# Kernel optimization log

Measured on AMD Instinct MI355X. Metric: run time of the kernel, lower is better.

Reference implementation:

```python
import jax, jax.numpy as jnp
import numpy as np

N_NODES = 60
N_EDGES = 1800
BATCH = 8192
NEG_SLOPE = 0.2  # PyG GATConv default leaky_relu slope


def _conv2d(x, w, b):
    y = jax.lax.conv_general_dilated(x, w, window_strides=(1, 1), padding='VALID',
                                     dimension_numbers=('NCHW', 'OIHW', 'NCHW'))
    return y + b[None, :, None, None]


def _maxpool2(x):
    return jax.lax.reduce_window(x, -jnp.inf, jax.lax.max, (1, 1, 2, 2), (1, 1, 2, 2), 'VALID')


def _gat(x, src, dst, edge_attr, W, a_src, a_dst, We, a_edge, b, n):
    # PyG GATConv, heads=1: xl = x W ; alpha_e = leakyrelu(a_src.xl[src] + a_dst.xl[dst] + a_edge.(edge_attr We))
    xl = x @ W                                    # [N, out]
    asrc = (xl * a_src).sum(-1)                   # [N]
    adst = (xl * a_dst).sum(-1)                   # [N]
    aedge = ((edge_attr @ We) * a_edge).sum(-1)   # [E]
    alpha = jax.nn.leaky_relu(asrc[src] + adst[dst] + aedge, NEG_SLOPE)
    # softmax over incoming edges of each dst node
    m = jax.ops.segment_max(alpha, dst, num_segments=n)
    ex = jnp.exp(alpha - m[dst])
    denom = jax.ops.segment_sum(ex, dst, num_segments=n)
    w_e = ex / denom[dst]
    out = jax.ops.segment_sum(w_e[:, None] * xl[src], dst, num_segments=n)
    return out + b


def _batchnorm_gnn(x):
    # torch code uses .item(): mean/std are detached python floats
    avg = jax.lax.stop_gradient(x.mean())
    std = jax.lax.stop_gradient(jnp.sqrt(((x - avg) ** 2).mean()))
    return (x - avg) / std


def setup_inputs() -> dict:
    key = jax.random.key(0)
    ks = jax.random.split(key, 24)
    f = lambda k, shape, scale=0.1: (jax.random.normal(k, shape, dtype=jnp.float32) * scale)
    inp = {
        'node_fea': jax.random.normal(ks[0], (N_NODES, 1), dtype=jnp.float32),
        'edge_fea': jax.random.normal(ks[1], (N_EDGES, 1), dtype=jnp.float32),
        'pic_fea': jax.random.normal(ks[2], (BATCH, 3, 32, 32), dtype=jnp.float32),
        'conv1_w': f(ks[3], (6, 3, 5, 5)), 'conv1_b': f(ks[4], (6,)),
        'conv2_w': f(ks[5], (16, 6, 5, 5)), 'conv2_b': f(ks[6], (16,)),
        'gat1_w': f(ks[7], (1, 6), 0.5), 'gat1_att_src': f(ks[8], (6,), 0.5),
        'gat1_att_dst': f(ks[9], (6,), 0.5), 'gat1_lin_edge': f(ks[10], (1, 6), 0.5),
        'gat1_att_edge': f(ks[11], (6,), 0.5), 'gat1_b': f(ks[12], (6,)),
        'gat2_w': f(ks[13], (6, 16), 0.3), 'gat2_att_src': f(ks[14], (16,), 0.3),
        'gat2_att_dst': f(ks[15], (16,), 0.3), 'gat2_lin_edge': f(ks[16], (1, 16), 0.3),
        'gat2_att_edge': f(ks[17], (16,), 0.3), 'gat2_b': f(ks[18], (16,)),
        'fc1_w': f(ks[19], (1360, 512), 0.03), 'fc1_b': f(ks[20], (512,)),
        'fc2_w': f(ks[21], (512, 10), 0.05), 'fc2_b': f(ks[22], (10,)),
        'edge_index': jax.random.randint(ks[23], (2, N_EDGES), 0, N_NODES, dtype=jnp.int64 if jax.config.jax_enable_x64 else jnp.int32),
    }
    return inp


def reference(node_fea, edge_fea, pic_fea,
              conv1_w, conv1_b, conv2_w, conv2_b,
              gat1_w, gat1_att_src, gat1_att_dst, gat1_lin_edge, gat1_att_edge, gat1_b,
              gat2_w, gat2_att_src, gat2_att_dst, gat2_lin_edge, gat2_att_edge, gat2_b,
              fc1_w, fc1_b, fc2_w, fc2_b, edge_index):
    n = node_fea.shape[0]
    # CNN branch: 32 -> 28 -> 14 -> 10 -> 5
    p = _maxpool2(jax.nn.relu(_conv2d(pic_fea, conv1_w, conv1_b)))
    p = _maxpool2(jax.nn.relu(_conv2d(p, conv2_w, conv2_b)))
    p = p.reshape(p.shape[0], -1)  # [B, 400]
    # add self loops (PyG default, fill_value='mean' for edge_attr)
    loop = jnp.arange(n)
    src = jnp.concatenate([edge_index[0], loop])
    dst = jnp.concatenate([edge_index[1], loop])
    ea = jnp.concatenate([edge_fea, jnp.broadcast_to(edge_fea.mean(0, keepdims=True), (n, edge_fea.shape[1]))], axis=0)
    # GNN branch
    x = _gat(node_fea, src, dst, ea, gat1_w, gat1_att_src, gat1_att_dst, gat1_lin_edge, gat1_att_edge, gat1_b, n)
    x = jax.nn.relu(_batchnorm_gnn(x))
    x = _gat(x, src, dst, ea, gat2_w, gat2_att_src, gat2_att_dst, gat2_lin_edge, gat2_att_edge, gat2_b, n)
    x = jax.nn.relu(_batchnorm_gnn(x))
    g = x.reshape(-1)  # [960]
    feat = jnp.concatenate([jnp.broadcast_to(g, (p.shape[0], g.shape[0])), p], axis=1)  # [B, 1360]
    h = jax.nn.relu(feat @ fc1_w + fc1_b)
    return jnp.tanh(h @ fc2_w + fc2_b)
```

## Files before the change

### kernel.cpp

```cpp
#include <hip/hip_runtime.h>
#include <math.h>

#define N_NODES 60
#define N_EDGES 1800
#define N_ETOT  1860
#define SLOPE   0.2f

struct ConvS {
    float simg[2 * 3 * 32 * 32];
    float c1[2 * 6 * 14 * 16];
    float pad[16];
};
struct GnnS {
    float ea[N_ETOT];
    float alpha[N_ETOT];
    float x_in[960];
    float xl[960];
    float outb[960];
    float as_[N_NODES], ad_[N_NODES], den_[N_NODES];
    float red[256];
    unsigned char srcs[N_ETOT], dsts[N_ETOT];
    unsigned short csr[N_ETOT];
    int cnt[N_NODES], off[N_NODES + 4];
};
union SMem { ConvS c; GnnS g; };

__device__ __forceinline__ void block_reduce_sum(float v, float* red, float* out) {
    int tid = threadIdx.x;
    red[tid] = v;
    __syncthreads();
    for (int st = 128; st > 0; st >>= 1) {
        if (tid < st) red[tid] += red[tid + st];
        __syncthreads();
    }
    *out = red[0];
    __syncthreads();
}

__device__ void gat_layer(GnnS& S, const float* x_in, int in_dim, int out_dim,
                          const float* W, const float* a_src, const float* a_dst,
                          const float* We, const float* a_edge, const float* bias,
                          float* xl, float* outb) {
    const int tid = threadIdx.x, nt = blockDim.x;
    for (int idx = tid; idx < N_NODES * out_dim; idx += nt) {
        int i = idx / out_dim, j = idx % out_dim;
        float s = 0.f;
        for (int k = 0; k < in_dim; ++k) s += x_in[i * in_dim + k] * W[k * out_dim + j];
        xl[idx] = s;
    }
    __syncthreads();
    for (int i = tid; i < N_NODES; i += nt) {
        float s = 0.f, d = 0.f;
        for (int j = 0; j < out_dim; ++j) {
            s += xl[i * out_dim + j] * a_src[j];
            d += xl[i * out_dim + j] * a_dst[j];
        }
        S.as_[i] = s; S.ad_[i] = d;
    }
    float ecoef = 0.f;
    for (int j = 0; j < out_dim; ++j) ecoef += We[j] * a_edge[j];
    __syncthreads();
    for (int e = tid; e < N_ETOT; e += nt) {
        float a = S.as_[S.srcs[e]] + S.ad_[S.dsts[e]] + S.ea[e] * ecoef;
        S.alpha[e] = (a >= 0.f) ? a : SLOPE * a;
    }
    __syncthreads();
    for (int d = tid; d < N_NODES; d += nt) {
        float m = -INFINITY;
        for (int k = S.off[d]; k < S.off[d + 1]; ++k) m = fmaxf(m, S.alpha[S.csr[k]]);
        float den = 0.f;
        for (int k = S.off[d]; k < S.off[d + 1]; ++k) {
            int e = S.csr[k];
            float ex = expf(S.alpha[e] - m);
            S.alpha[e] = ex;
            den += ex;
        }
        S.den_[d] = den;
    }
    __syncthreads();
    for (int idx = tid; idx < N_NODES * out_dim; idx += nt) {
        int d = idx / out_dim, j = idx % out_dim;
        float s = 0.f;
        for (int k = S.off[d]; k < S.off[d + 1]; ++k) {
            int e = S.csr[k];
            s += S.alpha[e] * xl[(int)S.srcs[e] * out_dim + j];
        }
        outb[idx] = s / S.den_[d] + bias[j];
    }
    __syncthreads();
}

__device__ void bn_relu(GnnS& S, const float* v, float* dst, int n) {
    const int tid = threadIdx.x, nt = blockDim.x;
    float s = 0.f;
    for (int i = tid; i < n; i += nt) s += v[i];
    float tot;
    block_reduce_sum(s, S.red, &tot);
    float avg = tot / n;
    float s2 = 0.f;
    for (int i = tid; i < n; i += nt) { float d = v[i] - avg; s2 += d * d; }
    block_reduce_sum(s2, S.red, &tot);
    float stdv = sqrtf(tot / n);
    for (int i = tid; i < n; i += nt) dst[i] = fmaxf((v[i] - avg) / stdv, 0.f);
    __syncthreads();
}

__device__ void gnn_path(GnnS& S,
    const float* node_fea, const float* edge_fea, const int* eidx,
    const float* g1w, const float* g1as, const float* g1ad,
    const float* g1we, const float* g1ae, const float* g1b,
    const float* g2w, const float* g2as, const float* g2ad,
    const float* g2we, const float* g2ae, const float* g2b,
    const float* fc1w, const float* fc1b, float* gcontrib) {
    const int tid = threadIdx.x, nt = blockDim.x;
    float s = 0.f;
    for (int e = tid; e < N_EDGES; e += nt) s += edge_fea[e];
    float tot;
    block_reduce_sum(s, S.red, &tot);
    float emean = tot / N_EDGES;
    for (int e = tid; e < N_ETOT; e += nt) {
        if (e < N_EDGES) {
            S.ea[e] = edge_fea[e];
            S.srcs[e] = (unsigned char)eidx[e];
            S.dsts[e] = (unsigned char)eidx[N_EDGES + e];
        } else {
            S.ea[e] = emean;
            S.srcs[e] = (unsigned char)(e - N_EDGES);
            S.dsts[e] = (unsigned char)(e - N_EDGES);
        }
    }
    if (tid < N_NODES) S.x_in[tid] = node_fea[tid];
    __syncthreads();
    if (tid < N_NODES) {
        int c = 0;
        for (int e = 0; e < N_ETOT; ++e) c += (S.dsts[e] == tid);
        S.cnt[tid] = c;
    }
    __syncthreads();
    if (tid == 0) {
        S.off[0] = 0;
        for (int d = 0; d < N_NODES; ++d) S.off[d + 1] = S.off[d] + S.cnt[d];
    }
    __syncthreads();
    if (tid < N_NODES) {
        int k = S.off[tid];
        for (int e = 0; e < N_ETOT; ++e)
            if (S.dsts[e] == tid) S.csr[k++] = (unsigned short)e;
    }
    __syncthreads();

    gat_layer(S, S.x_in, 1, 6, g1w, g1as, g1ad, g1we, g1ae, g1b, S.xl, S.outb);
    bn_relu(S, S.outb, S.x_in, N_NODES * 6);
    gat_layer(S, S.x_in, 6, 16, g2w, g2as, g2ad, g2we, g2ae, g2b, S.xl, S.outb);
    bn_relu(S, S.outb, S.x_in, N_NODES * 16);

    for (int j = tid; j < 512; j += nt) {
        float acc = fc1b[j];
#pragma unroll 4
        for (int k = 0; k < 960; ++k) acc += S.x_in[k] * fc1w[(size_t)k * 512 + j];
        gcontrib[j] = acc;
    }
}

__device__ void conv_path(ConvS& C, int img0,
                          const float* __restrict__ pic,
                          const float* __restrict__ w1, const float* __restrict__ b1,
                          const float* __restrict__ w2, const float* __restrict__ b2,
                          float* __restrict__ p) {
    const int tid = threadIdx.x;
    const int w = tid >> 6, lane = tid & 63;

    {
        const float4* src = (const float4*)(pic + (size_t)img0 * 3072);
        float4* dst = (float4*)C.simg;
        for (int i = tid; i < 1536; i += 256) dst[i] = src[i];
    }
    __syncthreads();

    {
        const int img = w >> 1, half = w & 1;
        const int y_rel = lane >> 5, x = lane & 31;
        const float* S = C.simg + img * 3072;
        float acc[7][6];
#pragma unroll
        for (int j = 0; j < 7; ++j)
#pragma unroll
            for (int oc = 0; oc < 6; ++oc) acc[j][oc] = b1[oc];

#pragma unroll 1
        for (int ic = 0; ic < 3; ++ic)
#pragma unroll 1
            for (int ky = 0; ky < 5; ++ky) {
                float wv[6][5];
#pragma unroll
                for (int oc = 0; oc < 6; ++oc)
#pragma unroll
                    for (int kx = 0; kx < 5; ++kx)
                        wv[oc][kx] = w1[(oc * 3 + ic) * 25 + ky * 5 + kx];
                const float* Sc = S + ic * 1024 + x;
#pragma unroll
                for (int j = 0; j < 7; ++j) {
                    int row = 2 * (half + 2 * j) + y_rel + ky;
                    const float* rp = Sc + row * 32;
                    float v0 = rp[0], v1 = rp[1], v2 = rp[2], v3 = rp[3], v4 = rp[4];
#pragma unroll
                    for (int oc = 0; oc < 6; ++oc)
                        acc[j][oc] += v0 * wv[oc][0] + v1 * wv[oc][1] + v2 * wv[oc][2]
                                    + v3 * wv[oc][3] + v4 * wv[oc][4];
                }
            }
#pragma unroll
        for (int j = 0; j < 7; ++j) {
            int yp = half + 2 * j;
#pragma unroll
            for (int oc = 0; oc < 6; ++oc) {
                float v = acc[j][oc];
                v = fmaxf(v, __shfl_xor(v, 1, 64));
                v = fmaxf(v, __shfl_xor(v, 32, 64));
                v = fmaxf(v, 0.f);
                if (y_rel == 0 && (x & 1) == 0 && x < 28)
                    C.c1[((img * 6 + oc) * 14 + yp) * 16 + (x >> 1)] = v;
            }
        }
    }
    __syncthreads();

    {
        const int img = w >> 1, och = w & 1;
        const int y_rel = lane >> 4, x = lane & 15;
        const float* C1 = C.c1 + img * (6 * 14 * 16);
        float acc[3][8];
#pragma unroll
        for (int t = 0; t < 3; ++t)
#pragma unroll
            for (int o = 0; o < 8; ++o) acc[t][o] = b2[och * 8 + o];

#pragma unroll 1
        for (int ic = 0; ic < 6; ++ic)
#pragma unroll 1
            for (int ky = 0; ky < 5; ++ky) {
                float wv[8][5];
#pragma unroll
                for (int o = 0; o < 8; ++o)
#pragma unroll
                    for (int kx = 0; kx < 5; ++kx)
                        wv[o][kx] = w2[((och * 8 + o) * 6 + ic) * 25 + ky * 5 + kx];
                const float* Cc = C1 + ic * 224 + x;
#pragma unroll
                for (int t = 0; t < 3; ++t) {
                    int row = 4 * t + y_rel + ky;
                    row = (row < 14) ? row : 13;
                    const float* rp = Cc + row * 16;
                    float v0 = rp[0], v1 = rp[1], v2 = rp[2], v3 = rp[3], v4 = rp[4];
#pragma unroll
                    for (int o = 0; o < 8; ++o)
                        acc[t][o] += v0 * wv[o][0] + v1 * wv[o][1] + v2 * wv[o][2]
                                   + v3 * wv[o][3] + v4 * wv[o][4];
                }
            }
#pragma unroll
        for (int t = 0; t < 3; ++t) {
#pragma unroll
            for (int o = 0; o < 8; ++o) {
                float v = acc[t][o];
                v = fmaxf(v, __shfl_xor(v, 1, 64));
                v = fmaxf(v, __shfl_xor(v, 16, 64));
                v = fmaxf(v, 0.f);
                int py = 2 * t + (y_rel >> 1);
                if ((y_rel & 1) == 0 && (x & 1) == 0 && x < 10 && py < 5) {
                    int oc = och * 8 + o;
                    p[((size_t)(img0 + img) * 16 + oc) * 25 + py * 5 + (x >> 1)] = v;
                }
            }
        }
    }
}

__global__ void __launch_bounds__(256, 4) fused_kernel(
    const float* __restrict__ node_fea, const float* __restrict__ edge_fea,
    const int* __restrict__ eidx,
    const float* g1w, const float* g1as, const float* g1ad,
    const float* g1we, const float* g1ae, const float* g1b,
    const float* g2w, const float* g2as, const float* g2ad,
    const float* g2we, const float* g2ae, const float* g2b,
    const float* __restrict__ fc1w, const float* __restrict__ fc1b,
    float* __restrict__ gcontrib,
    const float* __restrict__ pic,
    const float* __restrict__ c1w, const float* __restrict__ c1b,
    const float* __restrict__ c2w, const float* __restrict__ c2b,
    float* __restrict__ p) {
    __shared__ SMem u;
    if (blockIdx.x == 0) {
        gnn_path(u.g, node_fea, edge_fea, eidx,
                 g1w, g1as, g1ad, g1we, g1ae, g1b,
                 g2w, g2as, g2ad, g2we, g2ae, g2b,
                 fc1w, fc1b, gcontrib);
    } else {
        conv_path(u.c, (blockIdx.x - 1) * 2, pic, c1w, c1b, c2w, c2b, p);
    }
}

#define FC1_ROWS 16
__global__ void fc1_kernel(
    const float* __restrict__ p, const float* __restrict__ w,
    const float* __restrict__ gcontrib, float* __restrict__ h) {
    __shared__ float sp[FC1_ROWS * 400];
    const int tid = threadIdx.x;
    const size_t r0 = (size_t)blockIdx.x * FC1_ROWS;
    for (int i = tid; i < FC1_ROWS * 400; i += 256) sp[i] = p[r0 * 400 + i];
    __syncthreads();
    const int c0 = tid, c1 = tid + 256;
    float acc[FC1_ROWS][2];
#pragma unroll
    for (int r = 0; r < FC1_ROWS; ++r) { acc[r][0] = 0.f; acc[r][1] = 0.f; }
    for (int k = 0; k < 400; k += 4) {
        float wa0 = w[(size_t)(k + 0) * 512 + c0], wa1 = w[(size_t)(k + 0) * 512 + c1];
        float wb0 = w[(size_t)(k + 1) * 512 + c0], wb1 = w[(size_t)(k + 1) * 512 + c1];
        float wc0 = w[(size_t)(k + 2) * 512 + c0], wc1 = w[(size_t)(k + 2) * 512 + c1];
        float wd0 = w[(size_t)(k + 3) * 512 + c0], wd1 = w[(size_t)(k + 3) * 512 + c1];
#pragma unroll
        for (int r = 0; r < FC1_ROWS; ++r) {
            float4 pv = *(const float4*)&sp[r * 400 + k];
            acc[r][0] += pv.x * wa0 + pv.y * wb0 + pv.z * wc0 + pv.w * wd0;
            acc[r][1] += pv.x * wa1 + pv.y * wb1 + pv.z * wc1 + pv.w * wd1;
        }
    }
    float g0 = gcontrib[c0], g1 = gcontrib[c1];
#pragma unroll
    for (int r = 0; r < FC1_ROWS; ++r) {
        h[(r0 + r) * 512 + c0] = fmaxf(acc[r][0] + g0, 0.f);
        h[(r0 + r) * 512 + c1] = fmaxf(acc[r][1] + g1, 0.f);
    }
}

__global__ void fc2_kernel(
    const float* __restrict__ h, const float* __restrict__ w,
    const float* __restrict__ b, float* __restrict__ out) {
    const int wave = threadIdx.x >> 6, lane = threadIdx.x & 63;
    const size_t row = (size_t)blockIdx.x * 4 + wave;
    const float* hr = h + row * 512;
    float partial[10];
#pragma unroll
    for (int j = 0; j < 10; ++j) partial[j] = 0.f;
    for (int k = lane; k < 512; k += 64) {
        float hv = hr[k];
        const float* wr = w + (size_t)k * 10;
#pragma unroll
        for (int j = 0; j < 10; ++j) partial[j] += hv * wr[j];
    }
#pragma unroll
    for (int j = 0; j < 10; ++j) {
        float v = partial[j];
        for (int sft = 32; sft > 0; sft >>= 1) v += __shfl_xor(v, sft, 64);
        partial[j] = v;
    }
    if (lane == 0) {
#pragma unroll
        for (int j = 0; j < 10; ++j)
            out[row * 10 + j] = tanhf(partial[j] + b[j]);
    }
}

extern "C" void kernel_launch(void* const* d_in, const int* in_sizes, int n_in,
                              void* d_out, int out_size, void* d_ws, size_t ws_size,
                              hipStream_t stream) {
    const float* node_fea = (const float*)d_in[0];
    const float* edge_fea = (const float*)d_in[1];
    const float* pic      = (const float*)d_in[2];
    const float* c1w = (const float*)d_in[3];
    const float* c1b = (const float*)d_in[4];
    const float* c2w = (const float*)d_in[5];
    const float* c2b = (const float*)d_in[6];
    const float* g1w  = (const float*)d_in[7];
    const float* g1as = (const float*)d_in[8];
    const float* g1ad = (const float*)d_in[9];
    const float* g1we = (const float*)d_in[10];
    const float* g1ae = (const float*)d_in[11];
    const float* g1b  = (const float*)d_in[12];
    const float* g2w  = (const float*)d_in[13];
    const float* g2as = (const float*)d_in[14];
    const float* g2ad = (const float*)d_in[15];
    const float* g2we = (const float*)d_in[16];
    const float* g2ae = (const float*)d_in[17];
    const float* g2b  = (const float*)d_in[18];
    const float* fc1w = (const float*)d_in[19];
    const float* fc1b = (const float*)d_in[20];
    const float* fc2w = (const float*)d_in[21];
    const float* fc2b = (const float*)d_in[22];
    const int*   eidx = (const int*)d_in[23];
    float* out = (float*)d_out;

    char* ws = (char*)d_ws;
    float* gcontrib = (float*)ws;
    float* p = (float*)(ws + 2048);
    float* h = (float*)(ws + 2048 + (size_t)8192 * 400 * 4);

    hipLaunchKernelGGL(fused_kernel, dim3(4097), dim3(256), 0, stream,
                       node_fea, edge_fea, eidx,
                       g1w, g1as, g1ad, g1we, g1ae, g1b,
                       g2w, g2as, g2ad, g2we, g2ae, g2b,
                       fc1w, fc1b, gcontrib,
                       pic, c1w, c1b, c2w, c2b, p);
    hipLaunchKernelGGL(fc1_kernel, dim3(8192 / FC1_ROWS), dim3(256), 0, stream,
                       p, fc1w + (size_t)960 * 512, gcontrib, h);
    hipLaunchKernelGGL(fc2_kernel, dim3(8192 / 4), dim3(256), 0, stream,
                       h, fc2w, fc2b, out);
}
```

Baseline: 426.9 us.

## Process one image per block with padded shared layout and 2-wide conv outputs

```diff
diff --git a/kernel.cpp b/kernel.cpp
--- a/kernel.cpp
+++ b/kernel.cpp
@@ -6,17 +6,19 @@
 #define N_ETOT  1860
 #define SLOPE   0.2f
 
+#define SROW 34
+#define SCH  (32 * SROW)
+#define CROW 18
+#define CCH  (14 * CROW)
 struct ConvS {
-    float simg[2 * 3 * 32 * 32];
-    float c1[2 * 6 * 14 * 16];
+    float simg[3 * SCH];
+    float c1[6 * CCH];
     float pad[16];
 };
 struct GnnS {
-    float ea[N_ETOT];
     float alpha[N_ETOT];
     float x_in[960];
     float xl[960];
-    float outb[960];
     float as_[N_NODES], ad_[N_NODES], den_[N_NODES];
     float red[256];
     unsigned char srcs[N_ETOT], dsts[N_ETOT];
@@ -40,6 +42,7 @@
 __device__ void gat_layer(GnnS& S, const float* x_in, int in_dim, int out_dim,
                           const float* W, const float* a_src, const float* a_dst,
                           const float* We, const float* a_edge, const float* bias,
+                          const float* edge_fea, float emean,
                           float* xl, float* outb) {
     const int tid = threadIdx.x, nt = blockDim.x;
     for (int idx = tid; idx < N_NODES * out_dim; idx += nt) {
@@ -61,7 +64,8 @@
     for (int j = 0; j < out_dim; ++j) ecoef += We[j] * a_edge[j];
     __syncthreads();
     for (int e = tid; e < N_ETOT; e += nt) {
-        float a = S.as_[S.srcs[e]] + S.ad_[S.dsts[e]] + S.ea[e] * ecoef;
+        float eaval = (e < N_EDGES) ? edge_fea[e] : emean;
+        float a = S.as_[S.srcs[e]] + S.ad_[S.dsts[e]] + eaval * ecoef;
         S.alpha[e] = (a >= 0.f) ? a : SLOPE * a;
     }
     __syncthreads();
@@ -90,7 +94,7 @@
     __syncthreads();
 }
 
-__device__ void bn_relu(GnnS& S, const float* v, float* dst, int n) {
+__device__ void bn_relu(GnnS& S, float* v, int n) {
     const int tid = threadIdx.x, nt = blockDim.x;
     float s = 0.f;
     for (int i = tid; i < n; i += nt) s += v[i];
@@ -101,7 +105,8 @@
     for (int i = tid; i < n; i += nt) { float d = v[i] - avg; s2 += d * d; }
     block_reduce_sum(s2, S.red, &tot);
     float stdv = sqrtf(tot / n);
-    for (int i = tid; i < n; i += nt) dst[i] = fmaxf((v[i] - avg) / stdv, 0.f);
+    __syncthreads();
+    for (int i = tid; i < n; i += nt) v[i] = fmaxf((v[i] - avg) / stdv, 0.f);
     __syncthreads();
 }
 
@@ -120,11 +125,9 @@
     float emean = tot / N_EDGES;
     for (int e = tid; e < N_ETOT; e += nt) {
         if (e < N_EDGES) {
-            S.ea[e] = edge_fea[e];
             S.srcs[e] = (unsigned char)eidx[e];
             S.dsts[e] = (unsigned char)eidx[N_EDGES + e];
         } else {
-            S.ea[e] = emean;
             S.srcs[e] = (unsigned char)(e - N_EDGES);
             S.dsts[e] = (unsigned char)(e - N_EDGES);
         }
@@ -149,10 +152,12 @@
     }
     __syncthreads();
 
-    gat_layer(S, S.x_in, 1, 6, g1w, g1as, g1ad, g1we, g1ae, g1b, S.xl, S.outb);
-    bn_relu(S, S.outb, S.x_in, N_NODES * 6);
-    gat_layer(S, S.x_in, 6, 16, g2w, g2as, g2ad, g2we, g2ae, g2b, S.xl, S.outb);
-    bn_relu(S, S.outb, S.x_in, N_NODES * 16);
+    gat_layer(S, S.x_in, 1, 6, g1w, g1as, g1ad, g1we, g1ae, g1b,
+              edge_fea, emean, S.xl, S.x_in);
+    bn_relu(S, S.x_in, N_NODES * 6);
+    gat_layer(S, S.x_in, 6, 16, g2w, g2as, g2ad, g2we, g2ae, g2b,
+              edge_fea, emean, S.xl, S.x_in);
+    bn_relu(S, S.x_in, N_NODES * 16);
 
     for (int j = tid; j < 512; j += nt) {
         float acc = fc1b[j];
@@ -162,7 +167,7 @@
     }
 }
 
-__device__ void conv_path(ConvS& C, int img0,
+__device__ void conv_path(ConvS& C, int img,
                           const float* __restrict__ pic,
                           const float* __restrict__ w1, const float* __restrict__ b1,
                           const float* __restrict__ w2, const float* __restrict__ b2,
@@ -170,22 +175,26 @@
     const int tid = threadIdx.x;
     const int w = tid >> 6, lane = tid & 63;
 
+    for (int i = tid; i < 768; i += 256) {
+        float4 v = ((const float4*)(pic + (size_t)img * 3072))[i];
+        int e = 4 * i, ic = e >> 10, rem = e & 1023, y = rem >> 5, x = rem & 31;
+        float2* dst = (float2*)&C.simg[ic * SCH + y * SROW + x];
+        dst[0] = make_float2(v.x, v.y);
+        dst[1] = make_float2(v.z, v.w);
+    }
+    __syncthreads();
+
     {
-        const float4* src = (const float4*)(pic + (size_t)img0 * 3072);
-        float4* dst = (float4*)C.simg;
-        for (int i = tid; i < 1536; i += 256) dst[i] = src[i];
-    }
-    __syncthreads();
-
-    {
-        const int img = w >> 1, half = w & 1;
-        const int y_rel = lane >> 5, x = lane & 31;
-        const float* S = C.simg + img * 3072;
-        float acc[7][6];
-#pragma unroll
-        for (int j = 0; j < 7; ++j)
-#pragma unroll
-            for (int oc = 0; oc < 6; ++oc) acc[j][oc] = b1[oc];
+        const int half = w & 1, jhalf = w >> 1;
+        const int jj = lane >> 5, y_rel = (lane >> 4) & 1, xp = lane & 15;
+        float acc[2][6][2];
+#pragma unroll
+        for (int jt = 0; jt < 2; ++jt)
+#pragma unroll
+            for (int oc = 0; oc < 6; ++oc) {
+                acc[jt][oc][0] = b1[oc];
+                acc[jt][oc][1] = b1[oc];
+            }
 
 #pragma unroll 1
         for (int ic = 0; ic < 3; ++ic)
@@ -197,86 +206,86 @@
 #pragma unroll
                     for (int kx = 0; kx < 5; ++kx)
                         wv[oc][kx] = w1[(oc * 3 + ic) * 25 + ky * 5 + kx];
-                const float* Sc = S + ic * 1024 + x;
-#pragma unroll
-                for (int j = 0; j < 7; ++j) {
-                    int row = 2 * (half + 2 * j) + y_rel + ky;
-                    const float* rp = Sc + row * 32;
-                    float v0 = rp[0], v1 = rp[1], v2 = rp[2], v3 = rp[3], v4 = rp[4];
-#pragma unroll
-                    for (int oc = 0; oc < 6; ++oc)
-                        acc[j][oc] += v0 * wv[oc][0] + v1 * wv[oc][1] + v2 * wv[oc][2]
-                                    + v3 * wv[oc][3] + v4 * wv[oc][4];
+#pragma unroll
+                for (int jt = 0; jt < 2; ++jt) {
+                    int j = 4 * jhalf + 2 * jt + jj;
+                    int jc = (j < 7) ? j : 6;
+                    int row = 4 * jc + 2 * half + y_rel + ky;
+                    const float2* rp = (const float2*)&C.simg[ic * SCH + row * SROW + 2 * xp];
+                    float2 A = rp[0], B = rp[1], D = rp[2];
+                    float w0 = A.x, w1v = A.y, w2v = B.x, w3 = B.y, w4 = D.x, w5 = D.y;
+#pragma unroll
+                    for (int oc = 0; oc < 6; ++oc) {
+                        acc[jt][oc][0] += w0 * wv[oc][0] + w1v * wv[oc][1] + w2v * wv[oc][2]
+                                        + w3 * wv[oc][3] + w4 * wv[oc][4];
+                        acc[jt][oc][1] += w1v * wv[oc][0] + w2v * wv[oc][1] + w3 * wv[oc][2]
+                                        + w4 * wv[oc][3] + w5 * wv[oc][4];
+                    }
                 }
             }
-#pragma unroll
-        for (int j = 0; j < 7; ++j) {
+        __syncthreads();
+#pragma unroll
+        for (int jt = 0; jt < 2; ++jt) {
+            int j = 4 * jhalf + 2 * jt + jj;
             int yp = half + 2 * j;
 #pragma unroll
             for (int oc = 0; oc < 6; ++oc) {
-                float v = acc[j][oc];
-                v = fmaxf(v, __shfl_xor(v, 1, 64));
-                v = fmaxf(v, __shfl_xor(v, 32, 64));
-                v = fmaxf(v, 0.f);
-                if (y_rel == 0 && (x & 1) == 0 && x < 28)
-                    C.c1[((img * 6 + oc) * 14 + yp) * 16 + (x >> 1)] = v;
+                float m = fmaxf(acc[jt][oc][0], acc[jt][oc][1]);
+                m = fmaxf(m, __shfl_xor(m, 16, 64));
+                m = fmaxf(m, 0.f);
+                if (y_rel == 0 && xp < 14 && j < 7)
+                    C.c1[oc * CCH + yp * CROW + xp] = m;
             }
         }
     }
     __syncthreads();
 
     {
-        const int img = w >> 1, och = w & 1;
-        const int y_rel = lane >> 4, x = lane & 15;
-        const float* C1 = C.c1 + img * (6 * 14 * 16);
-        float acc[3][8];
-#pragma unroll
-        for (int t = 0; t < 3; ++t)
-#pragma unroll
-            for (int o = 0; o < 8; ++o) acc[t][o] = b2[och * 8 + o];
+        const int y_pre = lane / 5, px = lane - 5 * y_pre;
+        const int ypc = (y_pre < 10) ? y_pre : 9;
+        float acc[4][2];
+#pragma unroll
+        for (int o = 0; o < 4; ++o) {
+            acc[o][0] = b2[4 * w + o];
+            acc[o][1] = b2[4 * w + o];
+        }
 
 #pragma unroll 1
         for (int ic = 0; ic < 6; ++ic)
 #pragma unroll 1
             for (int ky = 0; ky < 5; ++ky) {
-                float wv[8][5];
-#pragma unroll
-                for (int o = 0; o < 8; ++o)
+                float wv[4][5];
+#pragma unroll
+                for (int o = 0; o < 4; ++o)
 #pragma unroll
                     for (int kx = 0; kx < 5; ++kx)
-                        wv[o][kx] = w2[((och * 8 + o) * 6 + ic) * 25 + ky * 5 + kx];
-                const float* Cc = C1 + ic * 224 + x;
-#pragma unroll
-                for (int t = 0; t < 3; ++t) {
-                    int row = 4 * t + y_rel + ky;
-                    row = (row < 14) ? row : 13;
-                    const float* rp = Cc + row * 16;
-                    float v0 = rp[0], v1 = rp[1], v2 = rp[2], v3 = rp[3], v4 = rp[4];
-#pragma unroll
-                    for (int o = 0; o < 8; ++o)
-                        acc[t][o] += v0 * wv[o][0] + v1 * wv[o][1] + v2 * wv[o][2]
-                                   + v3 * wv[o][3] + v4 * wv[o][4];
+                        wv[o][kx] = w2[((4 * w + o) * 6 + ic) * 25 + ky * 5 + kx];
+                int row = ypc + ky;
+                const float2* rp = (const float2*)&C.c1[ic * CCH + row * CROW + 2 * px];
+                float2 A = rp[0], B = rp[1], D = rp[2];
+                float w0 = A.x, w1v = A.y, w2v = B.x, w3 = B.y, w4 = D.x, w5 = D.y;
+#pragma unroll
+                for (int o = 0; o < 4; ++o) {
+                    acc[o][0] += w0 * wv[o][0] + w1v * wv[o][1] + w2v * wv[o][2]
+                               + w3 * wv[o][3] + w4 * wv[o][4];
+                    acc[o][1] += w1v * wv[o][0] + w2v * wv[o][1] + w3 * wv[o][2]
+                               + w4 * wv[o][3] + w5 * wv[o][4];
                 }
             }
 #pragma unroll
-        for (int t = 0; t < 3; ++t) {
-#pragma unroll
-            for (int o = 0; o < 8; ++o) {
-                float v = acc[t][o];
-                v = fmaxf(v, __shfl_xor(v, 1, 64));
-                v = fmaxf(v, __shfl_xor(v, 16, 64));
-                v = fmaxf(v, 0.f);
-                int py = 2 * t + (y_rel >> 1);
-                if ((y_rel & 1) == 0 && (x & 1) == 0 && x < 10 && py < 5) {
-                    int oc = och * 8 + o;
-                    p[((size_t)(img0 + img) * 16 + oc) * 25 + py * 5 + (x >> 1)] = v;
-                }
+        for (int o = 0; o < 4; ++o) {
+            float m = fmaxf(acc[o][0], acc[o][1]);
+            float pm = __shfl(m, lane + 5, 64);
+            m = fmaxf(fmaxf(m, pm), 0.f);
+            if (lane < 50 && (y_pre & 1) == 0) {
+                int py = y_pre >> 1;
+                p[((size_t)img * 16 + 4 * w + o) * 25 + py * 5 + px] = m;
             }
         }
     }
 }
 
-__global__ void __launch_bounds__(256, 4) fused_kernel(
+__global__ void __launch_bounds__(256, 6) fused_kernel(
     const float* __restrict__ node_fea, const float* __restrict__ edge_fea,
     const int* __restrict__ eidx,
     const float* g1w, const float* g1as, const float* g1ad,
@@ -296,7 +305,7 @@
                  g2w, g2as, g2ad, g2we, g2ae, g2b,
                  fc1w, fc1b, gcontrib);
     } else {
-        conv_path(u.c, (blockIdx.x - 1) * 2, pic, c1w, c1b, c2w, c2b, p);
+        conv_path(u.c, blockIdx.x - 1, pic, c1w, c1b, c2w, c2b, p);
     }
 }
 
@@ -395,7 +404,7 @@
     float* p = (float*)(ws + 2048);
     float* h = (float*)(ws + 2048 + (size_t)8192 * 400 * 4);
 
-    hipLaunchKernelGGL(fused_kernel, dim3(4097), dim3(256), 0, stream,
+    hipLaunchKernelGGL(fused_kernel, dim3(8193), dim3(256), 0, stream,
                        node_fea, edge_fea, eidx,
                        g1w, g1as, g1ad, g1we, g1ae, g1b,
                        g2w, g2as, g2ad, g2we, g2ae, g2b,
```

Measured after the change: 443.5 us. 3.9% more time.
